# Optimization experiments

Measured on AMD Instinct MI355X. Metric: run time of the kernel, lower is better.

Reference implementation:

```python
import jax, jax.numpy as jnp
import numpy as np

SIGMA = 1.0
RADIUS = int(4.0 * SIGMA + 0.5)  # scipy/skimage truncate=4.0

_t = np.arange(-RADIUS, RADIUS + 1, dtype=np.float32)
_w = np.exp(-0.5 * (_t / SIGMA) ** 2)
KERNEL = jnp.asarray(_w / _w.sum())  # [2*RADIUS+1]


def _blur_axis(x, axis):
    """1D Gaussian filter along `axis` with 'nearest' (edge) boundary."""
    pads = [(0, 0)] * x.ndim
    pads[axis] = (RADIUS, RADIUS)
    xp = jnp.pad(x, pads, mode='edge')
    n = x.shape[axis]
    out = KERNEL[0] * jax.lax.slice_in_dim(xp, 0, n, axis=axis)
    for k in range(1, 2 * RADIUS + 1):
        out = out + KERNEL[k] * jax.lax.slice_in_dim(xp, k, k + n, axis=axis)
    return out


def gaussian_blur(x):
    # skimage.filters.gaussian on each [T, F] sample: blur over both axes
    x = _blur_axis(x, axis=1)  # time axis
    x = _blur_axis(x, axis=2)  # feature axis
    return x


def lstm_last_hidden(x, W_ih, W_hh, b_ih, b_hh):
    B, T, F = x.shape
    H = W_hh.shape[1]
    # precompute input projections for all timesteps: [B, T, 4H]
    xg = jnp.einsum('btf,gf->btg', x, W_ih) + b_ih + b_hh
    xg = jnp.transpose(xg, (1, 0, 2))  # [T, B, 4H]

    def step(carry, xt):
        h, c = carry
        g = xt + h @ W_hh.T  # [B, 4H]
        i, f, gg, o = jnp.split(g, 4, axis=-1)  # torch gate order i,f,g,o
        i = jax.nn.sigmoid(i)
        f = jax.nn.sigmoid(f)
        gg = jnp.tanh(gg)
        o = jax.nn.sigmoid(o)
        c = f * c + i * gg
        h = o * jnp.tanh(c)
        return (h, c), None

    h0 = jnp.zeros((B, H), dtype=x.dtype)
    c0 = jnp.zeros((B, H), dtype=x.dtype)
    (h_last, _), _ = jax.lax.scan(step, (h0, c0), xg)
    return h_last  # [B, H]


def setup_inputs() -> dict:
    key = jax.random.key(0)
    ks = jax.random.split(key, 7)
    B, T, F, H, O = 64, 1024, 256, 1024, 256
    s_ih = 1.0 / np.sqrt(F)
    s_hh = 1.0 / np.sqrt(H)
    return {
        'x': jax.random.uniform(ks[0], (B, T, F), dtype=jnp.float32),
        'W_ih': jax.random.normal(ks[1], (4 * H, F), dtype=jnp.float32) * s_ih,
        'W_hh': jax.random.normal(ks[2], (4 * H, H), dtype=jnp.float32) * s_hh,
        'b_ih': jax.random.normal(ks[3], (4 * H,), dtype=jnp.float32) * s_hh,
        'b_hh': jax.random.normal(ks[4], (4 * H,), dtype=jnp.float32) * s_hh,
        'W_fc': jax.random.normal(ks[5], (O, H), dtype=jnp.float32) * s_hh,
        'b_fc': jax.random.normal(ks[6], (O,), dtype=jnp.float32) * s_hh,
    }


def reference(x, W_ih, W_hh, b_ih, b_hh, W_fc, b_fc):
    xb = gaussian_blur(x)
    h_last = lstm_last_hidden(xb, W_ih, W_hh, b_ih, b_hh)
    return h_last @ W_fc.T + b_fc  # [B, O]
```

## Files before the change

kernel.cpp:

```cpp
#include <hip/hip_runtime.h>

typedef __bf16 bf16x8 __attribute__((ext_vector_type(8)));
typedef float f32x4 __attribute__((ext_vector_type(4)));

#define T_STEPS 1024
#define H_SZ    1024
#define F_IN    256
#define NGROUP  4
#define NB      16
#define WPG     64

__device__ __forceinline__ unsigned short f2bf(float f) {
    union { float f; unsigned u; } v; v.f = f;
    unsigned r = v.u + 0x7fffu + ((v.u >> 16) & 1u);
    return (unsigned short)(r >> 16);
}

__device__ __forceinline__ float fsigmoid(float x) {
    return 1.0f / (1.0f + __expf(-x));
}
__device__ __forceinline__ float ftanh(float x) {
    return 1.0f - 2.0f / (__expf(2.0f * x) + 1.0f);
}

__global__ __launch_bounds__(256) void blur_kernel(
    const float* __restrict__ x, unsigned short* __restrict__ xb)
{
    __shared__ float tb[64][256];
    const float kk[9] = {
        0.000133831f, 0.0044318617f, 0.0539911273f, 0.2419714457f,
        0.3989434694f,
        0.2419714457f, 0.0539911273f, 0.0044318617f, 0.000133831f };

    const int b     = blockIdx.x >> 4;
    const int chunk = blockIdx.x & 15;
    const int t0    = chunk * 64;
    const int f     = threadIdx.x;
    const float* xbase = x + (size_t)b * T_STEPS * F_IN;

    for (int r = 0; r < 64; r++) {
        int t = t0 + r;
        float acc = 0.0f;
        #pragma unroll
        for (int d = 0; d < 9; d++) {
            int ts = t + d - 4;
            ts = min(max(ts, 0), T_STEPS - 1);
            acc += kk[d] * xbase[ts * F_IN + f];
        }
        tb[r][f] = acc;
    }
    __syncthreads();
    for (int r = 0; r < 64; r++) {
        float acc = 0.0f;
        #pragma unroll
        for (int d = 0; d < 9; d++) {
            int fs = f + d - 4;
            fs = min(max(fs, 0), F_IN - 1);
            acc += kk[d] * tb[r][fs];
        }
        xb[((size_t)b * T_STEPS + t0 + r) * F_IN + f] = f2bf(acc);
    }
}

__global__ __launch_bounds__(256, 1) void lstm_persist(
    const unsigned short* __restrict__ xb,
    const float* __restrict__ Whh,
    const float* __restrict__ Wih,
    const float* __restrict__ bih,
    const float* __restrict__ bhh,
    unsigned short* __restrict__ hbuf,
    unsigned int* __restrict__ arrive)
{
    const int wg   = blockIdx.x;
    const int grp  = wg >> 6;
    const int w    = wg & 63;
    const int tid  = threadIdx.x;
    const int q    = tid >> 6;
    const int lane = tid & 63;
    const int lrow = lane & 15;
    const int lq   = lane >> 4;

    __shared__ f32x4 part[4][4][64];

    bf16x8 wa[8][4];
    bf16x8 wx[2][4];
    const int row_lo = w * 16 + lrow;
    #pragma unroll
    for (int kt = 0; kt < 8; kt++) {
        const int kofs = q * 256 + kt * 32 + lq * 8;
        #pragma unroll
        for (int g = 0; g < 4; g++) {
            const float* src = Whh + (size_t)(g * H_SZ + row_lo) * H_SZ + kofs;
            union { bf16x8 v; unsigned short s[8]; } u;
            #pragma unroll
            for (int j = 0; j < 8; j++) u.s[j] = f2bf(src[j]);
            wa[kt][g] = u.v;
        }
    }
    #pragma unroll
    for (int kt = 0; kt < 2; kt++) {
        const int kofs = q * 64 + kt * 32 + lq * 8;
        #pragma unroll
        for (int g = 0; g < 4; g++) {
            const float* src = Wih + (size_t)(g * H_SZ + row_lo) * F_IN + kofs;
            union { bf16x8 v; unsigned short s[8]; } u;
            #pragma unroll
            for (int j = 0; j < 8; j++) u.s[j] = f2bf(src[j]);
            wx[kt][g] = u.v;
        }
    }

    const int uhid = tid & 15;
    const int ub   = tid >> 4;
    float bias[4];
    #pragma unroll
    for (int g = 0; g < 4; g++) {
        int r = g * H_SZ + w * 16 + uhid;
        bias[g] = bih[r] + bhh[r];
    }
    float c_reg = 0.0f;

    const int b_abs_l = grp * NB + lrow;
    const unsigned short* xrow_base =
        xb + ((size_t)b_abs_l * T_STEPS) * F_IN + q * 64 + lq * 8;
    unsigned short* hdst =
        hbuf + (size_t)(grp * NB + ub) * H_SZ + w * 16 + uhid;

    for (int t = 0; t < T_STEPS; t++) {
        const unsigned short* xrow = xrow_base + (size_t)t * F_IN;
        bf16x8 xf0 = *reinterpret_cast<const bf16x8*>(xrow);
        bf16x8 xf1 = *reinterpret_cast<const bf16x8*>(xrow + 32);

        const unsigned short* hprev =
            hbuf + ((size_t)((t & 1) ^ 1) * 64 + b_abs_l) * H_SZ
                 + q * 256 + lq * 8;
        bf16x8 hf0, hf1, hf2, hf3, hf4, hf5, hf6, hf7;
        asm volatile(
            "global_load_dwordx4 %0, %8, off sc0 sc1\n\t"
            "global_load_dwordx4 %1, %8, off offset:64 sc0 sc1\n\t"
            "global_load_dwordx4 %2, %8, off offset:128 sc0 sc1\n\t"
            "global_load_dwordx4 %3, %8, off offset:192 sc0 sc1\n\t"
            "global_load_dwordx4 %4, %8, off offset:256 sc0 sc1\n\t"
            "global_load_dwordx4 %5, %8, off offset:320 sc0 sc1\n\t"
            "global_load_dwordx4 %6, %8, off offset:384 sc0 sc1\n\t"
            "global_load_dwordx4 %7, %8, off offset:448 sc0 sc1\n\t"
            "s_waitcnt vmcnt(0)"
            : "=&v"(hf0), "=&v"(hf1), "=&v"(hf2), "=&v"(hf3),
              "=&v"(hf4), "=&v"(hf5), "=&v"(hf6), "=&v"(hf7)
            : "v"(hprev)
            : "memory");
        bf16x8 hfa[8] = { hf0, hf1, hf2, hf3, hf4, hf5, hf6, hf7 };

        f32x4 acc[4];
        #pragma unroll
        for (int g = 0; g < 4; g++) acc[g] = (f32x4){0.f, 0.f, 0.f, 0.f};
        #pragma unroll
        for (int kt = 0; kt < 8; kt++)
            #pragma unroll
            for (int g = 0; g < 4; g++)
                acc[g] = __builtin_amdgcn_mfma_f32_16x16x32_bf16(
                    wa[kt][g], hfa[kt], acc[g], 0, 0, 0);
        acc[0] = __builtin_amdgcn_mfma_f32_16x16x32_bf16(wx[0][0], xf0, acc[0], 0, 0, 0);
        acc[1] = __builtin_amdgcn_mfma_f32_16x16x32_bf16(wx[0][1], xf0, acc[1], 0, 0, 0);
        acc[2] = __builtin_amdgcn_mfma_f32_16x16x32_bf16(wx[0][2], xf0, acc[2], 0, 0, 0);
        acc[3] = __builtin_amdgcn_mfma_f32_16x16x32_bf16(wx[0][3], xf0, acc[3], 0, 0, 0);
        acc[0] = __builtin_amdgcn_mfma_f32_16x16x32_bf16(wx[1][0], xf1, acc[0], 0, 0, 0);
        acc[1] = __builtin_amdgcn_mfma_f32_16x16x32_bf16(wx[1][1], xf1, acc[1], 0, 0, 0);
        acc[2] = __builtin_amdgcn_mfma_f32_16x16x32_bf16(wx[1][2], xf1, acc[2], 0, 0, 0);
        acc[3] = __builtin_amdgcn_mfma_f32_16x16x32_bf16(wx[1][3], xf1, acc[3], 0, 0, 0);

        #pragma unroll
        for (int g = 0; g < 4; g++)
            part[q][g][lane] = acc[g];
        __syncthreads();

        float gv[4];
        #pragma unroll
        for (int g = 0; g < 4; g++) {
            float s = bias[g];
            #pragma unroll
            for (int qq = 0; qq < 4; qq++)
                s += part[qq][g][(uhid >> 2) * 16 + ub][uhid & 3];
            gv[g] = s;
        }
        float ig = fsigmoid(gv[0]);
        float fg = fsigmoid(gv[1]);
        float gg = ftanh(gv[2]);
        float og = fsigmoid(gv[3]);
        c_reg = fg * c_reg + ig * gg;
        float hv = og * ftanh(c_reg);

        unsigned short hb = f2bf(hv);
        unsigned short* dst = hdst + (size_t)(t & 1) * 64 * H_SZ;
        asm volatile(
            "global_store_short %0, %1, off sc0 sc1\n\t"
            "s_waitcnt vmcnt(0)"
            :: "v"(dst), "v"(hb)
            : "memory");
        __syncthreads();

        if (tid == 0) {
            unsigned int* ctr = &arrive[grp * T_STEPS + t];
            __hip_atomic_fetch_add(ctr, 1u, __ATOMIC_RELAXED,
                                   __HIP_MEMORY_SCOPE_AGENT);
            while (__hip_atomic_load(ctr, __ATOMIC_RELAXED,
                                     __HIP_MEMORY_SCOPE_AGENT) < (unsigned)WPG) {}
        }
        __syncthreads();
    }
}

__global__ __launch_bounds__(256) void final_fc(
    const unsigned short* __restrict__ hbuf,
    const float* __restrict__ Wfc, const float* __restrict__ bfc,
    float* __restrict__ out)
{
    __shared__ float hs[H_SZ];
    const int b = blockIdx.x;
    const unsigned short* hrow = hbuf + (size_t)64 * H_SZ + (size_t)b * H_SZ;
    for (int k = threadIdx.x; k < H_SZ; k += 256) {
        union { unsigned u; float f; } cv;
        cv.u = ((unsigned)hrow[k]) << 16;
        hs[k] = cv.f;
    }
    __syncthreads();
    const int o = threadIdx.x;
    const float4* wr = reinterpret_cast<const float4*>(Wfc + (size_t)o * H_SZ);
    float acc = bfc[o];
    for (int k4 = 0; k4 < H_SZ / 4; k4++) {
        float4 wv = wr[k4];
        acc += hs[k4 * 4 + 0] * wv.x + hs[k4 * 4 + 1] * wv.y
             + hs[k4 * 4 + 2] * wv.z + hs[k4 * 4 + 3] * wv.w;
    }
    out[(size_t)b * 256 + o] = acc;
}

extern "C" void kernel_launch(void* const* d_in, const int* in_sizes, int n_in,
                              void* d_out, int out_size, void* d_ws,
                              size_t ws_size, hipStream_t stream)
{
    (void)in_sizes; (void)n_in; (void)out_size; (void)ws_size;
    const float* x   = (const float*)d_in[0];
    const float* Wih = (const float*)d_in[1];
    const float* Whh = (const float*)d_in[2];
    const float* bih = (const float*)d_in[3];
    const float* bhh = (const float*)d_in[4];
    const float* Wfc = (const float*)d_in[5];
    const float* bfc = (const float*)d_in[6];
    float* out = (float*)d_out;

    char* ws = (char*)d_ws;
    unsigned short* xblur = (unsigned short*)ws;
    unsigned short* hbuf  = (unsigned short*)(ws + 33554432);
    unsigned int*   arrv  = (unsigned int*)(ws + 33554432 + 262144);

    hipMemsetAsync(hbuf, 0, 262144 + 16384, stream);

    blur_kernel<<<dim3(1024), dim3(256), 0, stream>>>(x, xblur);

    void* kargs[] = { (void*)&xblur, (void*)&Whh, (void*)&Wih,
                      (void*)&bih, (void*)&bhh, (void*)&hbuf, (void*)&arrv };
    hipLaunchCooperativeKernel((void*)lstm_persist, dim3(256), dim3(256),
                               kargs, 0, stream);

    final_fc<<<dim3(64), dim3(256), 0, stream>>>(hbuf, Wfc, bfc, out);
}
```

Measured before the change: 4.181 ms.

## Replace atomic-counter grid barrier with per-workgroup step flags and conflict-free reduction layout

Drops the per-step shared arrival counter, where one thread increments and spins. Each workgroup now publishes its completed step in its own flag word, and before reading h each lane polls the flags of the workgroups that produced its slice. This turns the all-to-all barrier into a distributed wait and removes one __syncthreads plus the atomic RMW contention. The LDS partial-sum buffer is also reindexed with a swizzled scalar layout to cut bank conflicts in the cross-wave reduction. The risks are memory-ordering subtleties with relaxed flags and a possible WAR hazard on the double-buffered hbuf, since a fast workgroup may overwrite the buffer before slow readers finish.

Result: slower. 5.113 ms (+22.3%).

```diff
diff --git a/kernel.cpp b/kernel.cpp
--- a/kernel.cpp
+++ b/kernel.cpp
@@ -21,6 +21,10 @@
 }
 __device__ __forceinline__ float ftanh(float x) {
     return 1.0f - 2.0f / (__expf(2.0f * x) + 1.0f);
+}
+
+__device__ __forceinline__ int redidx(int h, int b) {
+    return ((4 * h + b) & 31) + 32 * ((h >> 3) * 4 + (b >> 2));
 }
 
 __global__ __launch_bounds__(256) void blur_kernel(
@@ -69,7 +73,7 @@
     const float* __restrict__ bih,
     const float* __restrict__ bhh,
     unsigned short* __restrict__ hbuf,
-    unsigned int* __restrict__ arrive)
+    unsigned int* __restrict__ flags)
 {
     const int wg   = blockIdx.x;
     const int grp  = wg >> 6;
@@ -80,7 +84,7 @@
     const int lrow = lane & 15;
     const int lq   = lane >> 4;
 
-    __shared__ f32x4 part[4][4][64];
+    __shared__ float red[4][4][256];
 
     bf16x8 wa[8][4];
     bf16x8 wx[2][4];
@@ -126,10 +130,27 @@
     unsigned short* hdst =
         hbuf + (size_t)(grp * NB + ub) * H_SZ + w * 16 + uhid;
 
+    int wofs[4];
+    #pragma unroll
+    for (int e = 0; e < 4; e++) wofs[e] = redidx(lq * 4 + e, lrow);
+    const int rofs = redidx(uhid, ub);
+
+    const unsigned int* fpoll = flags + grp * WPG + q * 16 + lrow;
+    unsigned int*       fmine = flags + grp * WPG + w;
+
     for (int t = 0; t < T_STEPS; t++) {
         const unsigned short* xrow = xrow_base + (size_t)t * F_IN;
         bf16x8 xf0 = *reinterpret_cast<const bf16x8*>(xrow);
         bf16x8 xf1 = *reinterpret_cast<const bf16x8*>(xrow + 32);
+
+        {
+            const unsigned int tv = (unsigned)t;
+            for (;;) {
+                unsigned int v = __hip_atomic_load(
+                    fpoll, __ATOMIC_RELAXED, __HIP_MEMORY_SCOPE_AGENT);
+                if (__all((int)(v >= tv))) break;
+            }
+        }
 
         const unsigned short* hprev =
             hbuf + ((size_t)((t & 1) ^ 1) * 64 + b_abs_l) * H_SZ
@@ -171,7 +192,9 @@
 
         #pragma unroll
         for (int g = 0; g < 4; g++)
-            part[q][g][lane] = acc[g];
+            #pragma unroll
+            for (int e = 0; e < 4; e++)
+                red[q][g][wofs[e]] = acc[g][e];
         __syncthreads();
 
         float gv[4];
@@ -180,7 +203,7 @@
             float s = bias[g];
             #pragma unroll
             for (int qq = 0; qq < 4; qq++)
-                s += part[qq][g][(uhid >> 2) * 16 + ub][uhid & 3];
+                s += red[qq][g][rofs];
             gv[g] = s;
         }
         float ig = fsigmoid(gv[0]);
@@ -199,14 +222,9 @@
             : "memory");
         __syncthreads();
 
-        if (tid == 0) {
-            unsigned int* ctr = &arrive[grp * T_STEPS + t];
-            __hip_atomic_fetch_add(ctr, 1u, __ATOMIC_RELAXED,
-                                   __HIP_MEMORY_SCOPE_AGENT);
-            while (__hip_atomic_load(ctr, __ATOMIC_RELAXED,
-                                     __HIP_MEMORY_SCOPE_AGENT) < (unsigned)WPG) {}
-        }
-        __syncthreads();
+        if (tid == 0)
+            __hip_atomic_store(fmine, (unsigned)(t + 1),
+                               __ATOMIC_RELAXED, __HIP_MEMORY_SCOPE_AGENT);
     }
 }
 
@@ -252,14 +270,14 @@
     char* ws = (char*)d_ws;
     unsigned short* xblur = (unsigned short*)ws;
     unsigned short* hbuf  = (unsigned short*)(ws + 33554432);
-    unsigned int*   arrv  = (unsigned int*)(ws + 33554432 + 262144);
+    unsigned int*   flg   = (unsigned int*)(ws + 33554432 + 262144);
 
     hipMemsetAsync(hbuf, 0, 262144 + 16384, stream);
 
     blur_kernel<<<dim3(1024), dim3(256), 0, stream>>>(x, xblur);
 
     void* kargs[] = { (void*)&xblur, (void*)&Whh, (void*)&Wih,
-                      (void*)&bih, (void*)&bhh, (void*)&hbuf, (void*)&arrv };
+                      (void*)&bih, (void*)&bhh, (void*)&hbuf, (void*)&flg };
     hipLaunchCooperativeKernel((void*)lstm_persist, dim3(256), dim3(256),
                                kargs, 0, stream);
 
```
